# Optimization experiments

Hardware: AMD Instinct MI355X
Metric: run time of the kernel (lower is better)

Reference implementation:

```python
import jax, jax.numpy as jnp
import numpy as np

N_USERS = 100000   # n
N_ITEMS = 50000    # m
N_EDGES = 1000000  # observed user-item interactions
D = 64             # embedding dim
ALPHA = 1.0        # Rankformer alpha
CLAMP = 1e-6       # args.rankformer_clamp_value (min clamp on omega norm)


def setup_inputs() -> dict:
    key = jax.random.key(0)
    k1, k2, k3 = jax.random.split(key, 3)
    x = jax.random.normal(k1, (N_USERS + N_ITEMS, D), dtype=jnp.float32)
    u = jax.random.randint(k2, (N_EDGES,), 0, N_USERS, dtype=jnp.int64)
    i = jax.random.randint(k3, (N_EDGES,), 0, N_ITEMS, dtype=jnp.int64)
    return {"x": x, "u": u, "i": i}


def reference(x, u, i):
    seg = jax.ops.segment_sum
    n, m = N_USERS, N_ITEMS
    dt = x.dtype

    # degree of each user; duj = number of non-interacted items
    dui = seg(jnp.ones((u.shape[0],), dt), u, num_segments=n)
    duj = m - dui
    dui = jnp.maximum(dui, 1.0)[:, None]  # [n,1]
    duj = jnp.maximum(duj, 1.0)[:, None]  # [n,1]

    # F.normalize(x): row-wise L2 with eps=1e-12
    xn = x / jnp.maximum(jnp.linalg.norm(x, axis=1, keepdims=True), 1e-12)
    xu, xi = xn[:n], xn[n:]   # normalized user / item features
    vu, vi = x[:n], x[n:]     # raw (value) user / item features

    xi_e = xi[i]              # [E,d] gathered item features per edge
    vi_e = vi[i]
    xui = jnp.sum(xu[u] * xi_e, axis=1, keepdims=True)  # [E,1] edge scores

    sxi = seg(xi_e, u, num_segments=n)          # sum of pos-item x per user
    sxj = jnp.sum(xi, axis=0) - sxi             # rest (neg) sum
    svi = seg(vi_e, u, num_segments=n)
    svj = jnp.sum(vi, axis=0) - svi

    b_pos = jnp.sum(xu * sxi, axis=1, keepdims=True) / dui
    b_neg = jnp.sum(xu * sxj, axis=1, keepdims=True) / duj

    du1 = jnp.sum(xu * sxi, axis=1, keepdims=True) / dui - b_neg + ALPHA
    du2 = -jnp.sum(xu * sxj, axis=1, keepdims=True) / duj + b_pos + ALPHA

    di1 = (jnp.sum(xi * seg((xu / dui)[u], i, num_segments=m), axis=1, keepdims=True)
           + seg(((-b_neg + ALPHA) / dui)[u], i, num_segments=m))
    rest_x = jnp.sum(xu / duj, axis=0)[None, :] - seg((xu / duj)[u], i, num_segments=m)
    rest_b = (jnp.sum((b_pos + ALPHA) / duj, axis=0)[None, :]
              - seg(((b_pos + ALPHA) / duj)[u], i, num_segments=m))
    di2 = -jnp.sum(xi * rest_x, axis=1, keepdims=True) + rest_b

    A = seg(xui * vi_e, u, num_segments=n)      # [n,d]
    # xvi.sum(0): S[a,b] = sum_m vi[m,a]*xi[m,b]  (never materialize [m,d,d])
    S = jnp.einsum('ma,mb->ab', vi, xi)
    zu1 = A / dui - svi * (b_neg - ALPHA) / dui
    zu2 = (xu @ S - A) / duj - svj * (b_pos + ALPHA) / duj

    zi1 = (seg(xui * vu[u] / dui[u], i, num_segments=m)
           - seg((vu * (b_neg - ALPHA) / dui)[u], i, num_segments=m))
    # ((xu/duj) outer vu).sum(0): T[a,b] = sum_n (xu/duj)[n,a]*vu[n,b]
    T = jnp.einsum('na,nb->ab', xu / duj, vu)
    rest_v = (jnp.sum(vu * (b_pos + ALPHA) / duj, axis=0)[None, :]
              - seg((vu * (b_pos + ALPHA) / duj)[u], i, num_segments=m))
    zi2 = xi @ T - seg(xui * (vu / duj)[u], i, num_segments=m) - rest_v

    z = jnp.concatenate([zu1 + zu2, zi1 + zi2], axis=0)          # [n+m,d]
    d1 = jnp.maximum(jnp.concatenate([du1, di1], axis=0), CLAMP)  # [n+m,1]
    d2 = jnp.maximum(jnp.concatenate([du2, di2], axis=0), CLAMP)
    return z / (d1 + d2)
```

## Files before the change

### kernel.cpp

```cpp
#include <hip/hip_runtime.h>

#define NU 100000
#define NI 50000
#define DD 64
#define ALPHA_C 1.0f
#define EPS_CLAMP 1e-6f

typedef _Float16 h4 __attribute__((ext_vector_type(4)));

__device__ __forceinline__ float rsum16(float v) {
  v += __shfl_xor(v, 1, 64);
  v += __shfl_xor(v, 2, 64);
  v += __shfl_xor(v, 4, 64);
  v += __shfl_xor(v, 8, 64);
  return v;
}
__device__ __forceinline__ float xgrp2(float v) {
  v += __shfl_xor(v, 16, 64);
  v += __shfl_xor(v, 32, 64);
  return v;
}
__device__ __forceinline__ float wsum(float v) { return xgrp2(rsum16(v)); }

__global__ void k_norm_sums(const float* __restrict__ x, float* __restrict__ inv_norm,
                            float* __restrict__ nrm, h4* __restrict__ xnih,
                            h4* __restrict__ vuh,
                            float* __restrict__ sum_xi, float* __restrict__ sum_vi) {
  __shared__ float sx_s[DD], sv_s[DD];
  if (threadIdx.x < DD) { sx_s[threadIdx.x] = 0.f; sv_s[threadIdx.x] = 0.f; }
  __syncthreads();
  int lane = threadIdx.x & 63;
  int g = lane >> 4, c = lane & 15;
  int wid = blockIdx.x * 4 + (threadIdx.x >> 6);
  int nw  = gridDim.x * 4;
  float sx0=0,sx1=0,sx2=0,sx3=0, sv0=0,sv1=0,sv2=0,sv3=0;
  for (int rb = wid * 4; rb < NU + NI; rb += nw * 4) {
    int r = rb + g;
    const float4 v4 = *(const float4*)(x + (size_t)r * DD + 4 * c);
    float p = v4.x*v4.x + v4.y*v4.y + v4.z*v4.z + v4.w*v4.w;
    p = rsum16(p);
    float nc  = fmaxf(sqrtf(p), 1e-12f);
    float inv = 1.0f / nc;
    if (c == 0) inv_norm[r] = inv;
    if (r >= NU) {
      int j = r - NU;
      if (c == 0) nrm[j] = nc;
      float xn0 = v4.x*inv, xn1 = v4.y*inv, xn2 = v4.z*inv, xn3 = v4.w*inv;
      h4 hw = { (_Float16)xn0, (_Float16)xn1, (_Float16)xn2, (_Float16)xn3 };
      xnih[(size_t)j * 16 + c] = hw;
      sv0 += v4.x; sv1 += v4.y; sv2 += v4.z; sv3 += v4.w;
      sx0 += xn0;  sx1 += xn1;  sx2 += xn2;  sx3 += xn3;
    } else {
      h4 hw = { (_Float16)v4.x, (_Float16)v4.y, (_Float16)v4.z, (_Float16)v4.w };
      vuh[(size_t)r * 16 + c] = hw;
    }
  }
  atomicAdd(&sx_s[4*c+0], sx0); atomicAdd(&sx_s[4*c+1], sx1);
  atomicAdd(&sx_s[4*c+2], sx2); atomicAdd(&sx_s[4*c+3], sx3);
  atomicAdd(&sv_s[4*c+0], sv0); atomicAdd(&sv_s[4*c+1], sv1);
  atomicAdd(&sv_s[4*c+2], sv2); atomicAdd(&sv_s[4*c+3], sv3);
  __syncthreads();
  if (threadIdx.x < DD) {
    atomicAdd(&sum_xi[threadIdx.x], sx_s[threadIdx.x]);
    atomicAdd(&sum_vi[threadIdx.x], sv_s[threadIdx.x]);
  }
}

__global__ void k_count2(const int* __restrict__ u, const int* __restrict__ it,
                         int* __restrict__ du, int* __restrict__ di,
                         int* __restrict__ ru_, int* __restrict__ ri_, int E) {
  int t = blockIdx.x * blockDim.x + threadIdx.x;
  int stride = gridDim.x * blockDim.x;
  for (int e = t; e < E; e += stride) {
    ru_[e] = atomicAdd(&du[u[e]], 1);
    ri_[e] = atomicAdd(&di[it[e]], 1);
  }
}

__global__ void k_scan2(const int* __restrict__ cnt0, int n0, int* __restrict__ off0,
                        const int* __restrict__ cnt1, int n1, int* __restrict__ off1) {
  const int* cnt = blockIdx.x ? cnt1 : cnt0;
  int n          = blockIdx.x ? n1   : n0;
  int* off       = blockIdx.x ? off1 : off0;
  __shared__ int wsum_s[16];
  __shared__ int carry_s;
  int t = threadIdx.x, lane = t & 63, wv = t >> 6;
  if (t == 0) carry_s = 0;
  __syncthreads();
  for (int base = 0; base < n; base += 1024 * 8) {
    int v[8];
    int s = 0;
    int i0 = base + t * 8;
#pragma unroll
    for (int k = 0; k < 8; ++k) {
      int idx = i0 + k;
      v[k] = (idx < n) ? cnt[idx] : 0;
      s += v[k];
    }
    int incl = s;
#pragma unroll
    for (int d = 1; d < 64; d <<= 1) {
      int t2 = __shfl_up(incl, d, 64);
      if (lane >= d) incl += t2;
    }
    if (lane == 63) wsum_s[wv] = incl;
    __syncthreads();
    int woff = 0, total = 0;
#pragma unroll
    for (int w = 0; w < 16; ++w) {
      int ws_v = wsum_s[w];
      woff += (w < wv) ? ws_v : 0;
      total += ws_v;
    }
    int excl = carry_s + woff + incl - s;
#pragma unroll
    for (int k = 0; k < 8; ++k) {
      int idx = i0 + k;
      if (idx < n) off[idx] = excl;
      excl += v[k];
    }
    __syncthreads();
    if (t == 0) carry_s += total;
    __syncthreads();
  }
  if (t == 0) off[n] = carry_s;
}

#define GRID_OUT 256
#define GS_OUT 85
#define OCH 32
__global__ void k_fused_os(const float* __restrict__ x, const float* __restrict__ inv_norm,
                           const int* __restrict__ du, float* __restrict__ part,
                           const int* __restrict__ u, const int* __restrict__ it,
                           const int* __restrict__ ru_, const int* __restrict__ ri_,
                           const int* __restrict__ uoff, const int* __restrict__ ioff, int E,
                           int* __restrict__ uev, unsigned long long* __restrict__ iue) {
  __shared__ float rows_s[OCH * DD];
  __shared__ float w_s[OCH];
  if ((int)blockIdx.x >= GRID_OUT) {
    int bloc = (int)blockIdx.x - GRID_OUT;
    int nb = (int)gridDim.x - GRID_OUT;
    int t = bloc * blockDim.x + threadIdx.x;
    int stride = nb * blockDim.x;
    for (int e = t; e < E; e += stride) {
      int uu = __builtin_nontemporal_load(&u[e]);
      int ii = __builtin_nontemporal_load(&it[e]);
      int pu = uoff[uu] + __builtin_nontemporal_load(&ru_[e]);
      int pi = ioff[ii] + __builtin_nontemporal_load(&ri_[e]);
      __builtin_nontemporal_store(ii, &uev[pu]);
      unsigned long long packed = (unsigned long long)(unsigned)uu |
                                  ((unsigned long long)(unsigned)pu << 32);
      __builtin_nontemporal_store(packed, &iue[pi]);
    }
    return;
  }
  bool isT = (int)blockIdx.x >= GS_OUT;
  int bloc = isT ? (int)blockIdx.x - GS_OUT : (int)blockIdx.x;
  int nb   = isT ? (GRID_OUT - GS_OUT) : GS_OUT;
  int nrows = isT ? NU : NI;
  int row0  = isT ? 0 : NU;
  int t = threadIdx.x;
  int a0 = (t >> 4) << 2;
  int b0 = (t & 15) << 2;
  float acc[4][4];
#pragma unroll
  for (int i = 0; i < 4; ++i)
#pragma unroll
    for (int j = 0; j < 4; ++j) acc[i][j] = 0.f;
  int nch = (nrows + OCH - 1) / OCH;
  int limit = row0 + nrows;
  for (int ch = bloc; ch < nch; ch += nb) {
    int rbase = row0 + ch * OCH;
    __syncthreads();
    {
      const float4* src = (const float4*)(x + (size_t)rbase * DD);
      float4* dst = (float4*)rows_s;
      int r1 = rbase + (t >> 4);
      dst[t] = (r1 < limit) ? src[t] : make_float4(0.f, 0.f, 0.f, 0.f);
      int r2 = rbase + ((t + 256) >> 4);
      dst[t + 256] = (r2 < limit) ? src[t + 256] : make_float4(0.f, 0.f, 0.f, 0.f);
      if (t < OCH) {
        int r = rbase + t;
        float w = 0.f;
        if (r < limit) {
          w = inv_norm[r];
          if (isT) w /= fmaxf((float)NI - (float)du[r], 1.0f);
        }
        w_s[t] = w;
      }
    }
    __syncthreads();
#pragma unroll 8
    for (int r = 0; r < OCH; ++r) {
      float w = w_s[r];
      const float4 av = *(const float4*)(rows_s + r * DD + a0);
      const float4 bv = *(const float4*)(rows_s + r * DD + b0);
      float wa0 = av.x * w, wa1 = av.y * w, wa2 = av.z * w, wa3 = av.w * w;
      acc[0][0] += wa0 * bv.x; acc[0][1] += wa0 * bv.y; acc[0][2] += wa0 * bv.z; acc[0][3] += wa0 * bv.w;
      acc[1][0] += wa1 * bv.x; acc[1][1] += wa1 * bv.y; acc[1][2] += wa1 * bv.z; acc[1][3] += wa1 * bv.w;
      acc[2][0] += wa2 * bv.x; acc[2][1] += wa2 * bv.y; acc[2][2] += wa2 * bv.z; acc[2][3] += wa2 * bv.w;
      acc[3][0] += wa3 * bv.x; acc[3][1] += wa3 * bv.y; acc[3][2] += wa3 * bv.z; acc[3][3] += wa3 * bv.w;
    }
  }
  float* dst = part + (size_t)blockIdx.x * (DD * DD);
#pragma unroll
  for (int i = 0; i < 4; ++i)
    *(float4*)(dst + (size_t)(a0 + i) * DD + b0) =
        make_float4(acc[i][0], acc[i][1], acc[i][2], acc[i][3]);
}

__global__ void k_redST(const float* __restrict__ part,
                        float* __restrict__ Smat, float* __restrict__ Tmat) {
  int k = blockIdx.x * blockDim.x + threadIdx.x;
  if (k < DD * DD) {
    float s = 0.f;
    for (int b = 0; b < GS_OUT; ++b) s += part[(size_t)b * (DD * DD) + k];
    Smat[k] = s;
  } else {
    int kk = k - DD * DD;
    float s = 0.f;
    for (int b = GS_OUT; b < GRID_OUT; ++b) s += part[(size_t)b * (DD * DD) + kk];
    Tmat[kk] = s;
  }
}

__global__ void k_matvec(const float* __restrict__ x, const float* __restrict__ inv_norm,
                         const float* __restrict__ Smat, const float* __restrict__ Tmat,
                         float* __restrict__ out, int gU) {
  bool isI = (int)blockIdx.x >= gU;
  const float* M = isI ? Tmat : Smat;
  int row0  = isI ? NU : 0;
  int nrows = isI ? NI : NU;
  int bloc  = isI ? (int)blockIdx.x - gU : (int)blockIdx.x;
  int nb    = isI ? (int)gridDim.x - gU : gU;
  int lane = threadIdx.x & 63;
  float m_reg[DD];
#pragma unroll
  for (int a = 0; a < DD; ++a) m_reg[a] = M[a * DD + lane];
  int wid = bloc * (blockDim.x >> 6) + (threadIdx.x >> 6);
  int nw  = nb * (blockDim.x >> 6);
  for (int rr = wid; rr < nrows; rr += nw) {
    int r = row0 + rr;
    float v = x[(size_t)r * DD + lane] * inv_norm[r];
    float a0 = 0.f, a1 = 0.f, a2 = 0.f, a3 = 0.f;
#pragma unroll
    for (int a = 0; a < DD; a += 4) {
      a0 += __shfl(v, a)     * m_reg[a];
      a1 += __shfl(v, a + 1) * m_reg[a + 1];
      a2 += __shfl(v, a + 2) * m_reg[a + 2];
      a3 += __shfl(v, a + 3) * m_reg[a + 3];
    }
    out[(size_t)r * DD + lane] = (a0 + a1) + (a2 + a3);
  }
}

__global__ void k_user5(const float* __restrict__ x, const float* __restrict__ inv_norm,
                        const float* __restrict__ nrm, const h4* __restrict__ xnih,
                        const int* __restrict__ uoff, const int* __restrict__ uev,
                        const float* __restrict__ sum_xi, const float* __restrict__ sum_vi,
                        float* __restrict__ d_raw, float4* __restrict__ usc,
                        float* __restrict__ out,
                        float* __restrict__ Gx, float* __restrict__ Gv, float* __restrict__ Gb) {
  __shared__ float gx_s[DD], gv_s[DD], gb_s;
  if (threadIdx.x < DD) { gx_s[threadIdx.x] = 0.f; gv_s[threadIdx.x] = 0.f; }
  if (threadIdx.x == 0) gb_s = 0.f;
  __syncthreads();
  int lane = threadIdx.x & 63;
  int g = lane >> 4, c = lane & 15;
  float gmask = (g == 0) ? 1.f : 0.f;
  int wid = blockIdx.x * (blockDim.x >> 6) + (threadIdx.x >> 6);
  int nw  = gridDim.x * (blockDim.x >> 6);
  const float4 sx4  = *(const float4*)(sum_xi + 4 * c);
  const float4 svl4 = *(const float4*)(sum_vi + 4 * c);
  float gxa0=0,gxa1=0,gxa2=0,gxa3=0, gva0=0,gva1=0,gva2=0,gva3=0, gb=0.f;
  for (int uu = wid; uu < NU; uu += nw) {
    size_t ru = (size_t)uu * DD;
    int beg = uoff[uu], end2 = uoff[uu + 1];
    int deg = end2 - beg;
    float a1 = 1.0f / fmaxf((float)deg, 1.0f);
    float a2 = 1.0f / fmaxf((float)(NI - deg), 1.0f);
    float invu = inv_norm[uu];
    const float4 v4 = *(const float4*)(x + ru + 4 * c);
    float4 xu4 = make_float4(v4.x*invu, v4.y*invu, v4.z*invu, v4.w*invu);
    float Av0=0,Av1=0,Av2=0,Av3=0, sv0=0,sv1=0,sv2=0,sv3=0;
    float sA = 0.f;
    for (int base = beg; base < end2; base += 64) {
      int nb2 = end2 - base; if (nb2 > 64) nb2 = 64;
      int ii_l = 0; float nc_l = 0.f;
      if (lane < nb2) {
        ii_l = uev[base + lane];
        nc_l = nrm[ii_l];
      }
      for (int k0 = 0; k0 < nb2; k0 += 4) {
        int   ii = __shfl(ii_l, k0 + g);
        float nc = __shfl(nc_l, k0 + g);
        float f  = (k0 + g < nb2) ? 1.f : 0.f;
        h4 hv = xnih[(size_t)ii * 16 + c];
        float r0 = (float)hv.x, r1 = (float)hv.y, r2 = (float)hv.z, r3 = (float)hv.w;
        float p = xu4.x*r0 + xu4.y*r1 + xu4.z*r2 + xu4.w*r3;
        float d = f * rsum16(p);
        float w = d * nc;
        Av0 += w * r0; Av1 += w * r1; Av2 += w * r2; Av3 += w * r3;
        sv0 += nc * r0; sv1 += nc * r1; sv2 += nc * r2; sv3 += nc * r3;
        sA += d;
        if (c == 0 && k0 + g < nb2) d_raw[base + k0 + g] = d;
      }
    }
    sA  = xgrp2(sA);
    Av0 = xgrp2(Av0); Av1 = xgrp2(Av1); Av2 = xgrp2(Av2); Av3 = xgrp2(Av3);
    sv0 = xgrp2(sv0); sv1 = xgrp2(sv1); sv2 = xgrp2(sv2); sv3 = xgrp2(sv3);
    float bp = sA * a1;
    float pbn = xu4.x*sx4.x + xu4.y*sx4.y + xu4.z*sx4.z + xu4.w*sx4.w;
    float bn = (rsum16(pbn) - sA) * a2;
    float s1 = (ALPHA_C - bn) * a1;
    float s2 = (bp + ALPHA_C) * a2;
    if (lane == 0) usc[uu] = make_float4(a1, a2, s1, s2);
    const float4 xs4 = *(const float4*)(out + ru + 4 * c);
    float c12 = s1 + s2, a12 = a1 - a2;
    float rden = 1.0f / (2.0f * fmaxf(bp - bn + ALPHA_C, EPS_CLAMP));
    float o0 = (Av0 * a12 + sv0 * c12 + xs4.x * a2 - svl4.x * s2) * rden;
    float o1 = (Av1 * a12 + sv1 * c12 + xs4.y * a2 - svl4.y * s2) * rden;
    float o2 = (Av2 * a12 + sv2 * c12 + xs4.z * a2 - svl4.z * s2) * rden;
    float o3 = (Av3 * a12 + sv3 * c12 + xs4.w * a2 - svl4.w * s2) * rden;
    if (g == 0) *(float4*)(out + ru + 4 * c) = make_float4(o0, o1, o2, o3);
    float t2 = a2 * gmask, t3 = s2 * gmask;
    gxa0 += t2 * xu4.x; gxa1 += t2 * xu4.y; gxa2 += t2 * xu4.z; gxa3 += t2 * xu4.w;
    gva0 += t3 * v4.x;  gva1 += t3 * v4.y;  gva2 += t3 * v4.z;  gva3 += t3 * v4.w;
    if (lane == 0) gb += s2;
  }
  if (g == 0) {
    atomicAdd(&gx_s[4*c+0], gxa0); atomicAdd(&gx_s[4*c+1], gxa1);
    atomicAdd(&gx_s[4*c+2], gxa2); atomicAdd(&gx_s[4*c+3], gxa3);
    atomicAdd(&gv_s[4*c+0], gva0); atomicAdd(&gv_s[4*c+1], gva1);
    atomicAdd(&gv_s[4*c+2], gva2); atomicAdd(&gv_s[4*c+3], gva3);
  }
  if (lane == 0) atomicAdd(&gb_s, gb);
  __syncthreads();
  if (threadIdx.x < DD) {
    atomicAdd(&Gx[threadIdx.x], gx_s[threadIdx.x]);
    atomicAdd(&Gv[threadIdx.x], gv_s[threadIdx.x]);
  }
  if (threadIdx.x == 0) atomicAdd(Gb, gb_s);
}

__global__ void k_item5(const float* __restrict__ x, const float* __restrict__ inv_norm,
                        const h4* __restrict__ vuh,
                        const int* __restrict__ ioff, const uint2* __restrict__ iue,
                        const float* __restrict__ d_raw, const float4* __restrict__ usc,
                        const float* __restrict__ Gx, const float* __restrict__ Gv,
                        const float* __restrict__ Gb, float* __restrict__ out) {
  int lane = threadIdx.x & 63;
  int g = lane >> 4, c = lane & 15;
  int wid = blockIdx.x * (blockDim.x >> 6) + (threadIdx.x >> 6);
  int nw  = gridDim.x * (blockDim.x >> 6);
  const float4 Gx4 = *(const float4*)(Gx + 4 * c);
  const float4 Gv4 = *(const float4*)(Gv + 4 * c);
  float gb = *Gb;
  for (int j = wid; j < NI; j += nw) {
    int r = NU + j;
    size_t rr = (size_t)r * DD;
    float invi = inv_norm[r];
    const float4 vi4 = *(const float4*)(x + rr + 4 * c);
    float4 xi4 = make_float4(vi4.x*invi, vi4.y*invi, vi4.z*invi, vi4.w*invi);
    int beg = ioff[j], end2 = ioff[j + 1];
    float W0=0,W1=0,W2=0,W3=0, q1=0.f, q2=0.f;
    for (int base = beg; base < end2; base += 64) {
      int nb2 = end2 - base; if (nb2 > 64) nb2 = 64;
      int uu_l = 0; float glx = 0.f;
      if (lane < nb2) {
        uint2 m = iue[base + lane];
        uu_l = (int)m.x;
        float d = d_raw[m.y];
        float4 cc = usc[uu_l];
        float t1 = d * cc.x + cc.z;
        float t2 = d * cc.y - cc.w;
        q1 += t1; q2 += t2;
        glx = t1 - t2;
      }
      for (int k0 = 0; k0 < nb2; k0 += 4) {
        int   ua = __shfl(uu_l, k0 + g);
        float ge = __shfl(glx,  k0 + g);
        h4 hv = vuh[(size_t)ua * 16 + c];
        W0 += ge * (float)hv.x; W1 += ge * (float)hv.y;
        W2 += ge * (float)hv.z; W3 += ge * (float)hv.w;
      }
    }
    q1 = wsum(q1); q2 = wsum(q2);
    W0 = xgrp2(W0); W1 = xgrp2(W1); W2 = xgrp2(W2); W3 = xgrp2(W3);
    float pd = xi4.x*Gx4.x + xi4.y*Gx4.y + xi4.z*Gx4.z + xi4.w*Gx4.w;
    float di1 = q1;
    float di2 = -rsum16(pd) + q2 + gb;
    const float4 xt4 = *(const float4*)(out + rr + 4 * c);
    float rden = 1.0f / (fmaxf(di1, EPS_CLAMP) + fmaxf(di2, EPS_CLAMP));
    float o0 = (W0 + xt4.x - Gv4.x) * rden;
    float o1 = (W1 + xt4.y - Gv4.y) * rden;
    float o2 = (W2 + xt4.z - Gv4.z) * rden;
    float o3 = (W3 + xt4.w - Gv4.w) * rden;
    if (g == 0) *(float4*)(out + rr + 4 * c) = make_float4(o0, o1, o2, o3);
  }
}

extern "C" void kernel_launch(void* const* d_in, const int* in_sizes, int n_in,
                              void* d_out, int out_size, void* d_ws, size_t ws_size,
                              hipStream_t stream) {
  const float* x  = (const float*)d_in[0];
  const int*   u  = (const int*)d_in[1];
  const int*   it = (const int*)d_in[2];
  float* out = (float*)d_out;
  const int E = in_sizes[1];

  char* wsb = (char*)d_ws;
  size_t off = 0;
  auto alloc = [&](size_t elems) { void* p = wsb + off; off += elems * 4; return p; };

  int*   du     = (int*)alloc(100016);
  int*   di     = (int*)alloc(50016);
  float* sum_xi = (float*)alloc(64);
  float* sum_vi = (float*)alloc(64);
  float* Gx     = (float*)alloc(64);
  float* Gv     = (float*)alloc(64);
  float* Gb     = (float*)alloc(16);
  size_t zero_bytes = off;

  float* Smat   = (float*)alloc(4096);
  float* Tmat   = (float*)alloc(4096);
  float* part   = (float*)alloc((size_t)GRID_OUT * 4096);
  float*  inv_norm = (float*)alloc(150016);
  float*  nrm      = (float*)alloc(50016);
  h4*     xnih     = (h4*)alloc((size_t)NI * 32);
  h4*     vuh      = (h4*)alloc((size_t)NU * 32);
  int*    uoff     = (int*)alloc(100016);
  int*    ioff     = (int*)alloc(50016);
  int*    ru_      = (int*)alloc(1000000);
  int*    ri_      = (int*)alloc(1000000);
  int*    uev      = (int*)alloc(1000000);
  unsigned long long* iue = (unsigned long long*)alloc(2000000);
  float*  d_raw    = (float*)alloc(1000000);
  float4* usc      = (float4*)alloc(400000);

  hipMemsetAsync(d_ws, 0, zero_bytes, stream);

  k_norm_sums<<<1024, 256, 0, stream>>>(x, inv_norm, nrm, xnih, vuh, sum_xi, sum_vi);
  k_count2<<<2048, 256, 0, stream>>>(u, it, du, di, ru_, ri_, E);
  k_scan2<<<2, 1024, 0, stream>>>(du, NU, uoff, di, NI, ioff);
  k_fused_os<<<GRID_OUT + 4096, 256, 0, stream>>>(x, inv_norm, du, part,
                                                  u, it, ru_, ri_, uoff, ioff, E,
                                                  uev, iue);
  k_redST<<<32, 256, 0, stream>>>(part, Smat, Tmat);
  k_matvec<<<1536, 256, 0, stream>>>(x, inv_norm, Smat, Tmat, out, 1024);
  k_user5<<<2048, 256, 0, stream>>>(x, inv_norm, nrm, xnih, uoff, uev, sum_xi, sum_vi,
                                    d_raw, usc, out, Gx, Gv, Gb);
  k_item5<<<2048, 256, 0, stream>>>(x, inv_norm, vuh, ioff, (const uint2*)iue, d_raw, usc,
                                    Gx, Gv, Gb, out);
}
```

Measured before the change: 598.7 us.

## Fuse counting into norm kernel, shrink index arrays, precompute per-edge item terms

Merges the degree-counting atomics into the normalization kernel as extra blocks, saving one launch and letting the two run side by side. Rank and user-edge item index arrays shrink to 16-bit, which relies on degrees and item ids fitting in 65535. The user kernel now writes finished per-edge (t1, t2) float2 values, so the item kernel does one gather per edge instead of separate d_raw and usc lookups. Grid sizes for the user and item kernels are doubled, and nontemporal stores are replaced with plain stores.

After: 652.8 us. 9.0% more time.

```diff
diff --git a/kernel.cpp b/kernel.cpp
--- a/kernel.cpp
+++ b/kernel.cpp
@@ -22,17 +22,35 @@
 }
 __device__ __forceinline__ float wsum(float v) { return xgrp2(rsum16(v)); }
 
-__global__ void k_norm_sums(const float* __restrict__ x, float* __restrict__ inv_norm,
-                            float* __restrict__ nrm, h4* __restrict__ xnih,
-                            h4* __restrict__ vuh,
-                            float* __restrict__ sum_xi, float* __restrict__ sum_vi) {
+#define GN_NORM 1024
+__global__ void k_norm_count(const float* __restrict__ x, float* __restrict__ inv_norm,
+                             float* __restrict__ nrm, h4* __restrict__ xnih,
+                             h4* __restrict__ vuh,
+                             float* __restrict__ sum_xi, float* __restrict__ sum_vi,
+                             const int* __restrict__ u, const int* __restrict__ it,
+                             int* __restrict__ du, int* __restrict__ di,
+                             unsigned short* __restrict__ ru_, unsigned short* __restrict__ ri_,
+                             int E) {
+  if ((int)blockIdx.x >= GN_NORM) {
+    int bloc = (int)blockIdx.x - GN_NORM;
+    int nb = (int)gridDim.x - GN_NORM;
+    int t = bloc * blockDim.x + threadIdx.x;
+    int stride = nb * blockDim.x;
+    for (int e = t; e < E; e += stride) {
+      int uu = __builtin_nontemporal_load(&u[e]);
+      int ii = __builtin_nontemporal_load(&it[e]);
+      ru_[e] = (unsigned short)atomicAdd(&du[uu], 1);
+      ri_[e] = (unsigned short)atomicAdd(&di[ii], 1);
+    }
+    return;
+  }
   __shared__ float sx_s[DD], sv_s[DD];
   if (threadIdx.x < DD) { sx_s[threadIdx.x] = 0.f; sv_s[threadIdx.x] = 0.f; }
   __syncthreads();
   int lane = threadIdx.x & 63;
   int g = lane >> 4, c = lane & 15;
   int wid = blockIdx.x * 4 + (threadIdx.x >> 6);
-  int nw  = gridDim.x * 4;
+  int nw  = GN_NORM * 4;
   float sx0=0,sx1=0,sx2=0,sx3=0, sv0=0,sv1=0,sv2=0,sv3=0;
   for (int rb = wid * 4; rb < NU + NI; rb += nw * 4) {
     int r = rb + g;
@@ -66,17 +84,6 @@
   }
 }
 
-__global__ void k_count2(const int* __restrict__ u, const int* __restrict__ it,
-                         int* __restrict__ du, int* __restrict__ di,
-                         int* __restrict__ ru_, int* __restrict__ ri_, int E) {
-  int t = blockIdx.x * blockDim.x + threadIdx.x;
-  int stride = gridDim.x * blockDim.x;
-  for (int e = t; e < E; e += stride) {
-    ru_[e] = atomicAdd(&du[u[e]], 1);
-    ri_[e] = atomicAdd(&di[it[e]], 1);
-  }
-}
-
 __global__ void k_scan2(const int* __restrict__ cnt0, int n0, int* __restrict__ off0,
                         const int* __restrict__ cnt1, int n1, int* __restrict__ off1) {
   const int* cnt = blockIdx.x ? cnt1 : cnt0;
@@ -132,9 +139,11 @@
 __global__ void k_fused_os(const float* __restrict__ x, const float* __restrict__ inv_norm,
                            const int* __restrict__ du, float* __restrict__ part,
                            const int* __restrict__ u, const int* __restrict__ it,
-                           const int* __restrict__ ru_, const int* __restrict__ ri_,
+                           const unsigned short* __restrict__ ru_,
+                           const unsigned short* __restrict__ ri_,
                            const int* __restrict__ uoff, const int* __restrict__ ioff, int E,
-                           int* __restrict__ uev, unsigned long long* __restrict__ iue) {
+                           unsigned short* __restrict__ uev,
+                           unsigned long long* __restrict__ iue) {
   __shared__ float rows_s[OCH * DD];
   __shared__ float w_s[OCH];
   if ((int)blockIdx.x >= GRID_OUT) {
@@ -145,12 +154,11 @@
     for (int e = t; e < E; e += stride) {
       int uu = __builtin_nontemporal_load(&u[e]);
       int ii = __builtin_nontemporal_load(&it[e]);
-      int pu = uoff[uu] + __builtin_nontemporal_load(&ru_[e]);
-      int pi = ioff[ii] + __builtin_nontemporal_load(&ri_[e]);
-      __builtin_nontemporal_store(ii, &uev[pu]);
-      unsigned long long packed = (unsigned long long)(unsigned)uu |
-                                  ((unsigned long long)(unsigned)pu << 32);
-      __builtin_nontemporal_store(packed, &iue[pi]);
+      int pu = uoff[uu] + (int)__builtin_nontemporal_load(&ru_[e]);
+      int pi = ioff[ii] + (int)__builtin_nontemporal_load(&ri_[e]);
+      uev[pu] = (unsigned short)ii;
+      iue[pi] = (unsigned long long)(unsigned)uu |
+                ((unsigned long long)(unsigned)pu << 32);
     }
     return;
   }
@@ -254,12 +262,11 @@
   }
 }
 
-__global__ void k_user5(const float* __restrict__ x, const float* __restrict__ inv_norm,
+__global__ void k_user8(const float* __restrict__ x, const float* __restrict__ inv_norm,
                         const float* __restrict__ nrm, const h4* __restrict__ xnih,
-                        const int* __restrict__ uoff, const int* __restrict__ uev,
+                        const int* __restrict__ uoff, const unsigned short* __restrict__ uev,
                         const float* __restrict__ sum_xi, const float* __restrict__ sum_vi,
-                        float* __restrict__ d_raw, float4* __restrict__ usc,
-                        float* __restrict__ out,
+                        float2* __restrict__ te, float* __restrict__ out,
                         float* __restrict__ Gx, float* __restrict__ Gv, float* __restrict__ Gb) {
   __shared__ float gx_s[DD], gv_s[DD], gb_s;
   if (threadIdx.x < DD) { gx_s[threadIdx.x] = 0.f; gv_s[threadIdx.x] = 0.f; }
@@ -272,6 +279,7 @@
   int nw  = gridDim.x * (blockDim.x >> 6);
   const float4 sx4  = *(const float4*)(sum_xi + 4 * c);
   const float4 svl4 = *(const float4*)(sum_vi + 4 * c);
+  float* tex2 = (float*)te;
   float gxa0=0,gxa1=0,gxa2=0,gxa3=0, gva0=0,gva1=0,gva2=0,gva3=0, gb=0.f;
   for (int uu = wid; uu < NU; uu += nw) {
     size_t ru = (size_t)uu * DD;
@@ -283,14 +291,16 @@
     const float4 v4 = *(const float4*)(x + ru + 4 * c);
     float4 xu4 = make_float4(v4.x*invu, v4.y*invu, v4.z*invu, v4.w*invu);
     float Av0=0,Av1=0,Av2=0,Av3=0, sv0=0,sv1=0,sv2=0,sv3=0;
-    float sA = 0.f;
+    float sA = 0.f, dmine = 0.f;
+    bool multi = deg > 64;
     for (int base = beg; base < end2; base += 64) {
       int nb2 = end2 - base; if (nb2 > 64) nb2 = 64;
       int ii_l = 0; float nc_l = 0.f;
       if (lane < nb2) {
-        ii_l = uev[base + lane];
+        ii_l = (int)uev[base + lane];
         nc_l = nrm[ii_l];
       }
+      dmine = 0.f;
       for (int k0 = 0; k0 < nb2; k0 += 4) {
         int   ii = __shfl(ii_l, k0 + g);
         float nc = __shfl(nc_l, k0 + g);
@@ -303,8 +313,10 @@
         Av0 += w * r0; Av1 += w * r1; Av2 += w * r2; Av3 += w * r3;
         sv0 += nc * r0; sv1 += nc * r1; sv2 += nc * r2; sv3 += nc * r3;
         sA += d;
-        if (c == 0 && k0 + g < nb2) d_raw[base + k0 + g] = d;
-      }
+        float cand = __shfl(d, (lane & 3) << 4);
+        if ((lane & 60) == k0) dmine = cand;
+      }
+      if (multi && lane < nb2) tex2[2 * (size_t)(base + lane)] = dmine;
     }
     sA  = xgrp2(sA);
     Av0 = xgrp2(Av0); Av1 = xgrp2(Av1); Av2 = xgrp2(Av2); Av3 = xgrp2(Av3);
@@ -314,7 +326,14 @@
     float bn = (rsum16(pbn) - sA) * a2;
     float s1 = (ALPHA_C - bn) * a1;
     float s2 = (bp + ALPHA_C) * a2;
-    if (lane == 0) usc[uu] = make_float4(a1, a2, s1, s2);
+    if (!multi) {
+      if (lane < deg) te[beg + lane] = make_float2(dmine * a1 + s1, dmine * a2 - s2);
+    } else {
+      for (int k = beg + lane; k < end2; k += 64) {
+        float dv = tex2[2 * (size_t)k];
+        te[k] = make_float2(dv * a1 + s1, dv * a2 - s2);
+      }
+    }
     const float4 xs4 = *(const float4*)(out + ru + 4 * c);
     float c12 = s1 + s2, a12 = a1 - a2;
     float rden = 1.0f / (2.0f * fmaxf(bp - bn + ALPHA_C, EPS_CLAMP));
@@ -323,9 +342,9 @@
     float o2 = (Av2 * a12 + sv2 * c12 + xs4.z * a2 - svl4.z * s2) * rden;
     float o3 = (Av3 * a12 + sv3 * c12 + xs4.w * a2 - svl4.w * s2) * rden;
     if (g == 0) *(float4*)(out + ru + 4 * c) = make_float4(o0, o1, o2, o3);
-    float t2 = a2 * gmask, t3 = s2 * gmask;
-    gxa0 += t2 * xu4.x; gxa1 += t2 * xu4.y; gxa2 += t2 * xu4.z; gxa3 += t2 * xu4.w;
-    gva0 += t3 * v4.x;  gva1 += t3 * v4.y;  gva2 += t3 * v4.z;  gva3 += t3 * v4.w;
+    float t2m = a2 * gmask, t3m = s2 * gmask;
+    gxa0 += t2m * xu4.x; gxa1 += t2m * xu4.y; gxa2 += t2m * xu4.z; gxa3 += t2m * xu4.w;
+    gva0 += t3m * v4.x;  gva1 += t3m * v4.y;  gva2 += t3m * v4.z;  gva3 += t3m * v4.w;
     if (lane == 0) gb += s2;
   }
   if (g == 0) {
@@ -343,10 +362,11 @@
   if (threadIdx.x == 0) atomicAdd(Gb, gb_s);
 }
 
-__global__ void k_item5(const float* __restrict__ x, const float* __restrict__ inv_norm,
+__global__ void k_item8(const float* __restrict__ x, const float* __restrict__ inv_norm,
                         const h4* __restrict__ vuh,
-                        const int* __restrict__ ioff, const uint2* __restrict__ iue,
-                        const float* __restrict__ d_raw, const float4* __restrict__ usc,
+                        const int* __restrict__ ioff,
+                        const unsigned long long* __restrict__ iue,
+                        const float2* __restrict__ te,
                         const float* __restrict__ Gx, const float* __restrict__ Gv,
                         const float* __restrict__ Gb, float* __restrict__ out) {
   int lane = threadIdx.x & 63;
@@ -355,7 +375,7 @@
   int nw  = gridDim.x * (blockDim.x >> 6);
   const float4 Gx4 = *(const float4*)(Gx + 4 * c);
   const float4 Gv4 = *(const float4*)(Gv + 4 * c);
-  float gb = *Gb;
+  float gbv = *Gb;
   for (int j = wid; j < NI; j += nw) {
     int r = NU + j;
     size_t rr = (size_t)r * DD;
@@ -368,14 +388,12 @@
       int nb2 = end2 - base; if (nb2 > 64) nb2 = 64;
       int uu_l = 0; float glx = 0.f;
       if (lane < nb2) {
-        uint2 m = iue[base + lane];
-        uu_l = (int)m.x;
-        float d = d_raw[m.y];
-        float4 cc = usc[uu_l];
-        float t1 = d * cc.x + cc.z;
-        float t2 = d * cc.y - cc.w;
-        q1 += t1; q2 += t2;
-        glx = t1 - t2;
+        unsigned long long m = iue[base + lane];
+        uu_l = (int)(unsigned)m;
+        int pu = (int)(m >> 32);
+        float2 t = te[pu];
+        q1 += t.x; q2 += t.y;
+        glx = t.x - t.y;
       }
       for (int k0 = 0; k0 < nb2; k0 += 4) {
         int   ua = __shfl(uu_l, k0 + g);
@@ -389,7 +407,7 @@
     W0 = xgrp2(W0); W1 = xgrp2(W1); W2 = xgrp2(W2); W3 = xgrp2(W3);
     float pd = xi4.x*Gx4.x + xi4.y*Gx4.y + xi4.z*Gx4.z + xi4.w*Gx4.w;
     float di1 = q1;
-    float di2 = -rsum16(pd) + q2 + gb;
+    float di2 = -rsum16(pd) + q2 + gbv;
     const float4 xt4 = *(const float4*)(out + rr + 4 * c);
     float rden = 1.0f / (fmaxf(di1, EPS_CLAMP) + fmaxf(di2, EPS_CLAMP));
     float o0 = (W0 + xt4.x - Gv4.x) * rden;
@@ -431,25 +449,25 @@
   h4*     vuh      = (h4*)alloc((size_t)NU * 32);
   int*    uoff     = (int*)alloc(100016);
   int*    ioff     = (int*)alloc(50016);
-  int*    ru_      = (int*)alloc(1000000);
-  int*    ri_      = (int*)alloc(1000000);
-  int*    uev      = (int*)alloc(1000000);
+  unsigned short* ru_ = (unsigned short*)alloc(500000);
+  unsigned short* ri_ = (unsigned short*)alloc(500000);
+  unsigned short* uev = (unsigned short*)alloc(500000);
   unsigned long long* iue = (unsigned long long*)alloc(2000000);
-  float*  d_raw    = (float*)alloc(1000000);
-  float4* usc      = (float4*)alloc(400000);
+  float2* te       = (float2*)alloc(2000000);
 
   hipMemsetAsync(d_ws, 0, zero_bytes, stream);
 
-  k_norm_sums<<<1024, 256, 0, stream>>>(x, inv_norm, nrm, xnih, vuh, sum_xi, sum_vi);
-  k_count2<<<2048, 256, 0, stream>>>(u, it, du, di, ru_, ri_, E);
+  k_norm_count<<<GN_NORM + 1024, 256, 0, stream>>>(x, inv_norm, nrm, xnih, vuh,
+                                                   sum_xi, sum_vi,
+                                                   u, it, du, di, ru_, ri_, E);
   k_scan2<<<2, 1024, 0, stream>>>(du, NU, uoff, di, NI, ioff);
   k_fused_os<<<GRID_OUT + 4096, 256, 0, stream>>>(x, inv_norm, du, part,
                                                   u, it, ru_, ri_, uoff, ioff, E,
                                                   uev, iue);
   k_redST<<<32, 256, 0, stream>>>(part, Smat, Tmat);
   k_matvec<<<1536, 256, 0, stream>>>(x, inv_norm, Smat, Tmat, out, 1024);
-  k_user5<<<2048, 256, 0, stream>>>(x, inv_norm, nrm, xnih, uoff, uev, sum_xi, sum_vi,
-                                    d_raw, usc, out, Gx, Gv, Gb);
-  k_item5<<<2048, 256, 0, stream>>>(x, inv_norm, vuh, ioff, (const uint2*)iue, d_raw, usc,
+  k_user8<<<4096, 256, 0, stream>>>(x, inv_norm, nrm, xnih, uoff, uev, sum_xi, sum_vi,
+                                    te, out, Gx, Gv, Gb);
+  k_item8<<<4096, 256, 0, stream>>>(x, inv_norm, vuh, ioff, iue, te,
                                     Gx, Gv, Gb, out);
 }
```
